# Performance work log

Hardware: AMD Instinct MI355X
Metric: run time of the kernel (lower is better)

Reference implementation:

```python
import jax, jax.numpy as jnp
import numpy as np

N_SRC = 50000
N_DST = 50000
E = 800000
D = 64


def setup_inputs() -> dict:
    key = jax.random.key(0)
    k1, k2, k3, k4 = jax.random.split(key, 4)
    src_emb = jax.random.normal(k1, (N_SRC, D), dtype=jnp.float32)
    e_att = jax.random.uniform(k2, (E, 1), dtype=jnp.float32)
    src_idx = jax.random.randint(k3, (E,), 0, N_SRC, dtype=jnp.int64)
    dst_idx = jax.random.randint(k4, (E,), 0, N_DST, dtype=jnp.int64)
    return {"src_emb": src_emb, "e_att": e_att, "src_idx": src_idx, "dst_idx": dst_idx}


def reference(src_emb, e_att, src_idx, dst_idx):
    # DGL: fn.src_mul_edge('emb_o','att','msg') then fn.sum('msg','emb_n')
    # msg[e] = src_emb[src_idx[e]] * e_att[e]  -> scatter-sum into dst nodes
    msg = src_emb[src_idx] * e_att                      # [E, D]
    emb_n = jax.ops.segment_sum(msg, dst_idx, num_segments=N_DST)  # [N_DST, D]
    return emb_n
```

## Files before the change

kernel.cpp:

```cpp
#include <hip/hip_runtime.h>
#include <hip/hip_fp16.h>


#define D 64
#define CAP 64
#define OVF_CAP 65536
#define NPART 8

__global__ void __launch_bounds__(256)
scatter_conv_kernel(const int* __restrict__ dst_idx, const int* __restrict__ src_idx,
                    const float* __restrict__ e_att, int* __restrict__ cursor,
                    unsigned* __restrict__ payload,
                    int* __restrict__ ovf_count, int* __restrict__ ovf_list,
                    const float* __restrict__ src_emb, __half* __restrict__ emb_h,
                    const int* __restrict__ tag,
                    int E, int n_dst, int rpx, int epb4, int SB, int n4) {
    if ((int)blockIdx.x >= SB) {
        int i = (((int)blockIdx.x - SB) * 256 + threadIdx.x) * 2;
#pragma unroll
        for (int t = 0; t < 2; ++t) {
            int idx = i + t;
            if (idx < n4) {
                float4 v = ((const float4*)src_emb)[idx];
                ushort4 h;
                h.x = __half_as_ushort(__float2half(v.x));
                h.y = __half_as_ushort(__float2half(v.y));
                h.z = __half_as_ushort(__float2half(v.z));
                h.w = __half_as_ushort(__float2half(v.w));
                ((ushort4*)emb_h)[idx] = h;
            }
        }
        return;
    }

    const unsigned Vu = (unsigned)*tag;
    int x     = blockIdx.x & (NPART - 1);
    int chunk = blockIdx.x >> 3;
    int lo  = x * rpx;
    int hi  = min(lo + rpx, n_dst);
    unsigned span = (unsigned)(hi - lo);

    int E4 = E >> 2;
    int i0 = chunk * epb4;
    int i1 = min(i0 + epb4, E4);

    for (int i = i0 + threadIdx.x; i < i1; i += 256) {
        int4 d4 = ((const int4*)dst_idx)[i];
        bool m0 = (unsigned)(d4.x - lo) < span;
        bool m1 = (unsigned)(d4.y - lo) < span;
        bool m2 = (unsigned)(d4.z - lo) < span;
        bool m3 = (unsigned)(d4.w - lo) < span;
        if (!(m0 | m1 | m2 | m3)) continue;
        int4   s4 = ((const int4*)src_idx)[i];
        float4 a4 = ((const float4*)e_att)[i];
        int   dd[4] = {d4.x, d4.y, d4.z, d4.w};
        int   ss[4] = {s4.x, s4.y, s4.z, s4.w};
        float aa[4] = {a4.x, a4.y, a4.z, a4.w};
        bool  mm[4] = {m0, m1, m2, m3};
#pragma unroll
        for (int k = 0; k < 4; ++k) {
            if (!mm[k]) continue;
            int d = dd[k];
            unsigned p = (unsigned)atomicAdd(&cursor[d], 1) - Vu;
            unsigned pay = (unsigned)ss[k] |
                           ((unsigned)__half_as_ushort(__float2half(aa[k])) << 16);
            if (p < CAP) {
                payload[(size_t)d * CAP + p] = pay;
            } else {
                unsigned oi = (unsigned)atomicAdd(ovf_count, 1) - Vu;
                if (oi < OVF_CAP) ovf_list[oi] = 4 * i + k;
            }
        }
    }
    if (chunk == 0) {
        for (int e = (E4 << 2) + threadIdx.x; e < E; e += 256) {
            int d = dst_idx[e];
            if ((unsigned)(d - lo) >= span) continue;
            unsigned p = (unsigned)atomicAdd(&cursor[d], 1) - Vu;
            unsigned pay = (unsigned)src_idx[e] |
                           ((unsigned)__half_as_ushort(__float2half(e_att[e])) << 16);
            if (p < CAP) payload[(size_t)d * CAP + p] = pay;
            else { unsigned oi = (unsigned)atomicAdd(ovf_count, 1) - Vu;
                   if (oi < OVF_CAP) ovf_list[oi] = e; }
        }
    }
}

__global__ void __launch_bounds__(256)
gather4_kernel(const __half* __restrict__ emb_h,
               const unsigned* __restrict__ payload,
               int* __restrict__ cursor,
               const int* __restrict__ dst_idx, const int* __restrict__ src_idx,
               const float* __restrict__ e_att, const float* __restrict__ src_emb,
               const int* __restrict__ ovf_count, const int* __restrict__ ovf_list,
               const int* __restrict__ tag,
               float* __restrict__ out, int n_dst, int n_src, int rpx) {
    const unsigned Vu = (unsigned)*tag;
    int x    = blockIdx.x & (NPART - 1);
    int g    = blockIdx.x >> 3;
    int wv   = threadIdx.x >> 6;
    int lane = threadIdx.x & 63;
    int sub  = lane >> 4;
    int l15  = lane & 15;

    int local = g * 16 + (wv << 2) + sub;
    int w = x * rpx + local;
    bool rowvalid = (local < rpx) && (w < n_dst);

    int cn = rowvalid ? (int)((unsigned)cursor[w] - Vu) : 0;
    if (rowvalid && l15 == 0) cursor[w] = (int)Vu;
    int cnt = min(cn, CAP);
    int c32 = min(cnt, 32);

    uint2 pr = make_uint2(0u, 0u);
    if (rowvalid) pr = ((const uint2*)(payload + (size_t)w * CAP))[l15];

    int cmax = max(c32, __shfl_xor(c32, 16));
    cmax = max(cmax, __shfl_xor(cmax, 32));

    float4 acc = make_float4(0.f, 0.f, 0.f, 0.f);
    unsigned smax = (unsigned)(n_src - 1);
    for (int j = 0; j < cmax; j += 8) {
        int sb = (sub << 4) + (j >> 1);
        unsigned pv[8];
#pragma unroll
        for (int t = 0; t < 4; ++t) {
            pv[2 * t]     = (unsigned)__shfl((int)pr.x, sb + t);
            pv[2 * t + 1] = (unsigned)__shfl((int)pr.y, sb + t);
        }
        float    aw[8];
        unsigned sidx[8];
#pragma unroll
        for (int k = 0; k < 8; ++k) {
            bool valid = (j + k < c32);
            aw[k]   = valid ? __half2float(__ushort_as_half((unsigned short)(pv[k] >> 16)))
                            : 0.f;
            sidx[k] = valid ? min(pv[k] & 0xffffu, smax) : 0u;
        }
        uint2 h[8];
#pragma unroll
        for (int k = 0; k < 8; ++k)
            h[k] = ((const uint2*)(emb_h + (size_t)sidx[k] * D))[l15];
#pragma unroll
        for (int k = 0; k < 8; ++k) {
            __half2 h0 = *(__half2*)&h[k].x;
            __half2 h1 = *(__half2*)&h[k].y;
            acc.x = fmaf(__low2float(h0),  aw[k], acc.x);
            acc.y = fmaf(__high2float(h0), aw[k], acc.y);
            acc.z = fmaf(__low2float(h1),  aw[k], acc.z);
            acc.w = fmaf(__high2float(h1), aw[k], acc.w);
        }
    }

    if (rowvalid & (cnt > 32)) {
        for (int j = 32; j < cnt; ++j) {
            unsigned pv = payload[(size_t)w * CAP + j];
            float a = __half2float(__ushort_as_half((unsigned short)(pv >> 16)));
            unsigned s = min(pv & 0xffffu, smax);
            uint2 hh = ((const uint2*)(emb_h + (size_t)s * D))[l15];
            __half2 h0 = *(__half2*)&hh.x;
            __half2 h1 = *(__half2*)&hh.y;
            acc.x = fmaf(__low2float(h0),  a, acc.x);
            acc.y = fmaf(__high2float(h0), a, acc.y);
            acc.z = fmaf(__low2float(h1),  a, acc.z);
            acc.w = fmaf(__high2float(h1), a, acc.w);
        }
    }

    if (rowvalid) {
        if (cn > CAP) {
            int oc = (int)((unsigned)*ovf_count - Vu);
            if (oc > OVF_CAP) oc = OVF_CAP;
            for (int i = 0; i < oc; ++i) {
                int e = ovf_list[i];
                if (dst_idx[e] == w) {
                    float a = e_att[e];
                    int   s = src_idx[e];
                    float4 v = ((const float4*)(src_emb + (size_t)s * D))[l15];
                    acc.x = fmaf(v.x, a, acc.x);
                    acc.y = fmaf(v.y, a, acc.y);
                    acc.z = fmaf(v.z, a, acc.z);
                    acc.w = fmaf(v.w, a, acc.w);
                }
            }
        }
        ((float4*)(out + (size_t)w * D))[l15] = acc;
    }
}

__global__ void __launch_bounds__(256)
atomic_fallback_kernel(const float* __restrict__ src_emb, const float* __restrict__ e_att,
                       const int* __restrict__ src_idx, const int* __restrict__ dst_idx,
                       float* __restrict__ out, int E) {
    int tid  = blockIdx.x * blockDim.x + threadIdx.x;
    int e    = tid >> 4;
    int part = tid & 15;
    if (e >= E) return;
    int   s = src_idx[e];
    int   d = dst_idx[e];
    float a = e_att[e];
    float4 v = ((const float4*)src_emb)[(size_t)s * 16 + part];
    float* orow = out + (size_t)d * D + part * 4;
    atomicAdd(orow + 0, v.x * a);
    atomicAdd(orow + 1, v.y * a);
    atomicAdd(orow + 2, v.z * a);
    atomicAdd(orow + 3, v.w * a);
}

extern "C" void kernel_launch(void* const* d_in, const int* in_sizes, int n_in,
                              void* d_out, int out_size, void* d_ws, size_t ws_size,
                              hipStream_t stream) {
    const float* src_emb = (const float*)d_in[0];
    const float* e_att   = (const float*)d_in[1];
    const int*   src_idx = (const int*)d_in[2];
    const int*   dst_idx = (const int*)d_in[3];
    float*       out     = (float*)d_out;

    const int E     = in_sizes[2];
    const int n_dst = out_size / D;
    const int n_src = in_sizes[0] / D;

    size_t off_pay = (size_t)n_src * D / 2;
    size_t off_cur = off_pay + (size_t)n_dst * CAP;
    size_t off_ovf = off_cur + (size_t)n_dst;
    size_t off_lst = off_ovf + 1;
    size_t off_tag = (off_lst + OVF_CAP + 3) & ~(size_t)3;
    size_t need_ints = off_tag + 4;

    if (n_src <= 65536 && ws_size >= need_ints * sizeof(int)) {
        __half*   emb_h   = (__half*)d_ws;
        unsigned* payload = (unsigned*)d_ws + off_pay;
        int*      cursor  = (int*)d_ws + off_cur;
        int*      ovf_count = (int*)d_ws + off_ovf;
        int*      ovf_list  = (int*)d_ws + off_lst;
        int*      tag       = (int*)d_ws + off_tag;

        const int rpx = (n_dst + NPART - 1) / NPART;
        const int chunks = 512;
        const int SB = chunks * NPART;
        const int E4 = E >> 2;
        const int epb4 = (E4 + chunks - 1) / chunks;
        const int n4 = n_src * D / 4;
        const int CB = (n4 / 2 + 255) / 256;

        scatter_conv_kernel<<<SB + CB, 256, 0, stream>>>(
            dst_idx, src_idx, e_att, cursor, payload, ovf_count, ovf_list,
            src_emb, emb_h, tag, E, n_dst, rpx, epb4, SB, n4);

        const int gpb = (rpx + 15) / 16;
        gather4_kernel<<<gpb * NPART, 256, 0, stream>>>(
            emb_h, payload, cursor, dst_idx, src_idx, e_att, src_emb,
            ovf_count, ovf_list, tag, out, n_dst, n_src, rpx);
        return;
    }

    hipMemsetAsync(d_out, 0, (size_t)out_size * sizeof(float), stream);
    atomic_fallback_kernel<<<(E * 16 + 255) / 256, 256, 0, stream>>>(
        src_emb, e_att, src_idx, dst_idx, out, E);
}
```

Baseline: 126.7 us.

## Replace partitioned scatter scan with single-pass edge scatter using agent-scope stores

The scatter kernel no longer has each of 8 dst-range partitions rescan all edges. It now uses one block per 256 int4 edge groups and processes every edge exactly once, writing payloads with relaxed agent-scope atomic stores. This removes the 8x redundant reads of dst_idx. The cost is that cursor atomics and payload writes are now spread over all of memory instead of staying localized per partition, which may hurt L2 locality across XCDs. The gather kernel also clamps overflow indices, and the fast path now requires n_dst to be divisible by 4.

```diff
diff --git a/kernel.cpp b/kernel.cpp
--- a/kernel.cpp
+++ b/kernel.cpp
@@ -7,14 +7,18 @@
 #define OVF_CAP 65536
 #define NPART 8
 
+__device__ __forceinline__ void ag_store(unsigned* p, unsigned v) {
+    __hip_atomic_store(p, v, __ATOMIC_RELAXED, __HIP_MEMORY_SCOPE_AGENT);
+}
+
 __global__ void __launch_bounds__(256)
-scatter_conv_kernel(const int* __restrict__ dst_idx, const int* __restrict__ src_idx,
-                    const float* __restrict__ e_att, int* __restrict__ cursor,
-                    unsigned* __restrict__ payload,
-                    int* __restrict__ ovf_count, int* __restrict__ ovf_list,
-                    const float* __restrict__ src_emb, __half* __restrict__ emb_h,
-                    const int* __restrict__ tag,
-                    int E, int n_dst, int rpx, int epb4, int SB, int n4) {
+scatter_sp_kernel(const int* __restrict__ dst_idx, const int* __restrict__ src_idx,
+                  const float* __restrict__ e_att, unsigned* __restrict__ cursor,
+                  unsigned* __restrict__ payload,
+                  unsigned* __restrict__ ovfc, unsigned* __restrict__ ovfl,
+                  const float* __restrict__ src_emb, __half* __restrict__ emb_h,
+                  const unsigned* __restrict__ tag,
+                  int E, int SB, int n4) {
     if ((int)blockIdx.x >= SB) {
         int i = (((int)blockIdx.x - SB) * 256 + threadIdx.x) * 2;
 #pragma unroll
@@ -33,55 +37,39 @@
         return;
     }
 
-    const unsigned Vu = (unsigned)*tag;
-    int x     = blockIdx.x & (NPART - 1);
-    int chunk = blockIdx.x >> 3;
-    int lo  = x * rpx;
-    int hi  = min(lo + rpx, n_dst);
-    unsigned span = (unsigned)(hi - lo);
-
-    int E4 = E >> 2;
-    int i0 = chunk * epb4;
-    int i1 = min(i0 + epb4, E4);
-
-    for (int i = i0 + threadIdx.x; i < i1; i += 256) {
-        int4 d4 = ((const int4*)dst_idx)[i];
-        bool m0 = (unsigned)(d4.x - lo) < span;
-        bool m1 = (unsigned)(d4.y - lo) < span;
-        bool m2 = (unsigned)(d4.z - lo) < span;
-        bool m3 = (unsigned)(d4.w - lo) < span;
-        if (!(m0 | m1 | m2 | m3)) continue;
+    const unsigned Vu = *tag;
+    const int E4 = E >> 2;
+
+    for (int i = (int)blockIdx.x * 256 + threadIdx.x; i < E4; i += SB * 256) {
+        int4   d4 = ((const int4*)dst_idx)[i];
         int4   s4 = ((const int4*)src_idx)[i];
         float4 a4 = ((const float4*)e_att)[i];
         int   dd[4] = {d4.x, d4.y, d4.z, d4.w};
         int   ss[4] = {s4.x, s4.y, s4.z, s4.w};
         float aa[4] = {a4.x, a4.y, a4.z, a4.w};
-        bool  mm[4] = {m0, m1, m2, m3};
 #pragma unroll
         for (int k = 0; k < 4; ++k) {
-            if (!mm[k]) continue;
             int d = dd[k];
-            unsigned p = (unsigned)atomicAdd(&cursor[d], 1) - Vu;
+            unsigned p = atomicAdd(&cursor[d], 1u) - Vu;
             unsigned pay = (unsigned)ss[k] |
                            ((unsigned)__half_as_ushort(__float2half(aa[k])) << 16);
             if (p < CAP) {
-                payload[(size_t)d * CAP + p] = pay;
+                ag_store(&payload[(size_t)d * CAP + p], pay);
             } else {
-                unsigned oi = (unsigned)atomicAdd(ovf_count, 1) - Vu;
-                if (oi < OVF_CAP) ovf_list[oi] = 4 * i + k;
+                unsigned oi = atomicAdd(ovfc, 1u) - Vu;
+                if (oi < OVF_CAP) ag_store(&ovfl[oi], (unsigned)(4 * i + k));
             }
         }
     }
-    if (chunk == 0) {
+    if (blockIdx.x == 0) {
         for (int e = (E4 << 2) + threadIdx.x; e < E; e += 256) {
             int d = dst_idx[e];
-            if ((unsigned)(d - lo) >= span) continue;
-            unsigned p = (unsigned)atomicAdd(&cursor[d], 1) - Vu;
+            unsigned p = atomicAdd(&cursor[d], 1u) - Vu;
             unsigned pay = (unsigned)src_idx[e] |
                            ((unsigned)__half_as_ushort(__float2half(e_att[e])) << 16);
-            if (p < CAP) payload[(size_t)d * CAP + p] = pay;
-            else { unsigned oi = (unsigned)atomicAdd(ovf_count, 1) - Vu;
-                   if (oi < OVF_CAP) ovf_list[oi] = e; }
+            if (p < CAP) ag_store(&payload[(size_t)d * CAP + p], pay);
+            else { unsigned oi = atomicAdd(ovfc, 1u) - Vu;
+                   if (oi < OVF_CAP) ag_store(&ovfl[oi], (unsigned)e); }
         }
     }
 }
@@ -173,9 +161,10 @@
             if (oc > OVF_CAP) oc = OVF_CAP;
             for (int i = 0; i < oc; ++i) {
                 int e = ovf_list[i];
-                if (dst_idx[e] == w) {
-                    float a = e_att[e];
-                    int   s = src_idx[e];
+                unsigned ue = min((unsigned)e, (unsigned)(2147483647));
+                if ((unsigned)dst_idx[ue] == (unsigned)w) {
+                    float a = e_att[ue];
+                    int   s = src_idx[ue];
                     float4 v = ((const float4*)(src_emb + (size_t)s * D))[l15];
                     acc.x = fmaf(v.x, a, acc.x);
                     acc.y = fmaf(v.y, a, acc.y);
@@ -227,30 +216,30 @@
     size_t off_tag = (off_lst + OVF_CAP + 3) & ~(size_t)3;
     size_t need_ints = off_tag + 4;
 
-    if (n_src <= 65536 && ws_size >= need_ints * sizeof(int)) {
+    if (n_src <= 65536 && (n_dst & 3) == 0 && ws_size >= need_ints * sizeof(int)) {
         __half*   emb_h   = (__half*)d_ws;
         unsigned* payload = (unsigned*)d_ws + off_pay;
-        int*      cursor  = (int*)d_ws + off_cur;
-        int*      ovf_count = (int*)d_ws + off_ovf;
-        int*      ovf_list  = (int*)d_ws + off_lst;
-        int*      tag       = (int*)d_ws + off_tag;
+        unsigned* cursor  = (unsigned*)d_ws + off_cur;
+        unsigned* ovfc    = (unsigned*)d_ws + off_ovf;
+        unsigned* ovfl    = (unsigned*)d_ws + off_lst;
+        unsigned* tag     = (unsigned*)d_ws + off_tag;
 
         const int rpx = (n_dst + NPART - 1) / NPART;
-        const int chunks = 512;
-        const int SB = chunks * NPART;
-        const int E4 = E >> 2;
-        const int epb4 = (E4 + chunks - 1) / chunks;
-        const int n4 = n_src * D / 4;
+        const int E4  = E >> 2;
+        const int n4  = n_src * D / 4;
+
+        const int SB = (E4 + 255) / 256;
         const int CB = (n4 / 2 + 255) / 256;
 
-        scatter_conv_kernel<<<SB + CB, 256, 0, stream>>>(
-            dst_idx, src_idx, e_att, cursor, payload, ovf_count, ovf_list,
-            src_emb, emb_h, tag, E, n_dst, rpx, epb4, SB, n4);
+        scatter_sp_kernel<<<SB + CB, 256, 0, stream>>>(
+            dst_idx, src_idx, e_att, cursor, payload, ovfc, ovfl,
+            src_emb, emb_h, tag, E, SB, n4);
 
         const int gpb = (rpx + 15) / 16;
         gather4_kernel<<<gpb * NPART, 256, 0, stream>>>(
-            emb_h, payload, cursor, dst_idx, src_idx, e_att, src_emb,
-            ovf_count, ovf_list, tag, out, n_dst, n_src, rpx);
+            emb_h, payload, (int*)cursor, dst_idx, src_idx, e_att, src_emb,
+            (const int*)ovfc, (const int*)ovfl, (const int*)tag,
+            out, n_dst, n_src, rpx);
         return;
     }
 
```

Result: slower. 142.3 us (+12.3%).
